# Optimization experiments

Measured on AMD Instinct MI355X. Metric: run time of the kernel, lower is better.

## Reference

```python
import jax, jax.numpy as jnp
import numpy as np

B, T, M, H = 64, 256, 512, 256  # batch, seq_len, d_model, lstm hidden


def setup_inputs() -> dict:
    key = jax.random.key(0)
    ks = jax.random.split(key, 10)
    s = 0.05  # weight init scale
    return {
        "enc_inputs": jax.random.normal(ks[0], (B, T, M), jnp.float32),
        "y": jax.random.normal(ks[1], (B, T, 1), jnp.float32),
        "Wd_w": jax.random.normal(ks[2], (M, 2 * H), jnp.float32) * s,  # W_d: Linear(2H, M)
        "Wd_b": jnp.zeros((M,), jnp.float32),
        "Ud_w": jax.random.normal(ks[3], (M, M), jnp.float32) * s,      # U_d: Linear(M, M, bias=False)
        "vd_w": jax.random.normal(ks[4], (1, M), jnp.float32) * s,      # v_d: Linear(M, 1, bias=False)
        "wt_w": jax.random.normal(ks[5], (1, M + 1), jnp.float32) * s,  # w_tilda: Linear(M+1, 1)
        "wt_b": jnp.zeros((1,), jnp.float32),
        "Wih": jax.random.normal(ks[6], (4 * H, 1), jnp.float32) * s,   # LSTMCell input weights
        "Whh": jax.random.normal(ks[7], (4 * H, H), jnp.float32) * s,   # LSTMCell hidden weights
        "bih": jnp.zeros((4 * H,), jnp.float32),
        "bhh": jnp.zeros((4 * H,), jnp.float32),
    }


def reference(enc_inputs, y, Wd_w, Wd_b, Ud_w, vd_w, wt_w, wt_b, Wih, Whh, bih, bhh):
    # U_d(enc_inputs) is loop-invariant -> hoist (same math as recomputing each step)
    y1 = jnp.einsum('btm,nm->btn', enc_inputs, Ud_w)  # [B,T,M]

    def step(carry, y_t):
        d, s = carry  # d = h_{t-1} [B,H], s = c'_{t-1} [B,H]
        x1 = jnp.concatenate([d, s], axis=1) @ Wd_w.T + Wd_b          # [B,M]
        z1 = jnp.tanh(x1[:, None, :] + y1)                            # [B,T,M]
        l_it = jnp.einsum('btm,m->bt', z1, vd_w[0])                   # [B,T]
        beta = jax.nn.softmax(l_it, axis=1)                           # softmax over encoder steps
        c_t = jnp.einsum('bt,btm->bm', beta, enc_inputs)              # [B,M]
        y_tilda = jnp.concatenate([c_t, y_t], axis=1) @ wt_w.T + wt_b # [B,1]
        # torch LSTMCell: gate order i, f, g, o
        gates = y_tilda @ Wih.T + bih + d @ Whh.T + bhh               # [B,4H]
        i, f, g, o = jnp.split(gates, 4, axis=1)
        s_new = jax.nn.sigmoid(f) * s + jax.nn.sigmoid(i) * jnp.tanh(g)
        d_new = jax.nn.sigmoid(o) * jnp.tanh(s_new)
        return (d_new, s_new), c_t

    b = enc_inputs.shape[0]
    init = (jnp.zeros((b, H), enc_inputs.dtype), jnp.zeros((b, H), enc_inputs.dtype))
    _, cs = jax.lax.scan(step, init, jnp.swapaxes(y, 0, 1))  # cs: [T,B,M]
    return jnp.sum(cs, axis=0)  # tgt = sum_t c_t, [B,M]
```

## Files before the change

kernel.cpp:

```cpp
#include <hip/hip_runtime.h>

typedef unsigned short u16;
typedef __attribute__((ext_vector_type(8))) short short8v;
typedef __attribute__((ext_vector_type(4))) float f32x4;

#define NB 64
#define NT 256
#define NM 512
#define NH 256

#define K2 2.8853900817779268f
#define LOG2E 1.4426950408889634f

__device__ __forceinline__ float bf2f(u16 u) {
  union { unsigned i; float f; } c; c.i = ((unsigned)u) << 16; return c.f;
}
__device__ __forceinline__ u16 f2bf(float f) {
  union { float fv; unsigned i; } c; c.fv = f;
  unsigned i = c.i;
  return (u16)((i + 0x7fffu + ((i >> 16) & 1u)) >> 16);
}
__device__ __forceinline__ float tanh_fast(float x) {
  return 1.0f - 2.0f * __builtin_amdgcn_rcpf(1.0f + __builtin_amdgcn_exp2f(K2 * x));
}
__device__ __forceinline__ float sigmoid_fast(float x) {
  return __builtin_amdgcn_rcpf(1.0f + __builtin_amdgcn_exp2f(-LOG2E * x));
}
__device__ __forceinline__ float uload(const float* p) {
  return __hip_atomic_load(p, __ATOMIC_RELAXED, __HIP_MEMORY_SCOPE_SYSTEM);
}
__device__ __forceinline__ void ustore(float* p, float v) {
  __hip_atomic_store(p, v, __ATOMIC_RELAXED, __HIP_MEMORY_SCOPE_SYSTEM);
}

__global__ void convert_f32_bf16(const float* __restrict__ in, u16* __restrict__ out, int n) {
  int i = blockIdx.x * blockDim.x + threadIdx.x;
  if (i < n) out[i] = f2bf(in[i]);
}

__global__ __launch_bounds__(256) void gemm_y1(const u16* __restrict__ A,
                                               const u16* __restrict__ Bm,
                                               u16* __restrict__ C) {
  const int w = threadIdx.x >> 6;
  const int l = threadIdx.x & 63;
  const int kg = l >> 4;
  const int r16 = l & 15;
  const int rowbase = blockIdx.x * 64 + w * 16;
  const int colbase = blockIdx.y * 64;
  const u16* ap = A + (size_t)(rowbase + r16) * 512 + kg * 8;
  f32x4 acc0 = {0,0,0,0}, acc1 = {0,0,0,0}, acc2 = {0,0,0,0}, acc3 = {0,0,0,0};
  for (int k = 0; k < 512; k += 32) {
    short8v af = *(const short8v*)(ap + k);
    const u16* bp = Bm + (size_t)(colbase + r16) * 512 + kg * 8 + k;
    short8v b0 = *(const short8v*)(bp);
    short8v b1 = *(const short8v*)(bp + 16 * 512);
    short8v b2 = *(const short8v*)(bp + 32 * 512);
    short8v b3 = *(const short8v*)(bp + 48 * 512);
    acc0 = __builtin_amdgcn_mfma_f32_16x16x32_bf16(af, b0, acc0, 0, 0, 0);
    acc1 = __builtin_amdgcn_mfma_f32_16x16x32_bf16(af, b1, acc1, 0, 0, 0);
    acc2 = __builtin_amdgcn_mfma_f32_16x16x32_bf16(af, b2, acc2, 0, 0, 0);
    ac3:
    acc3 = __builtin_amdgcn_mfma_f32_16x16x32_bf16(af, b3, acc3, 0, 0, 0);
  }
  const int rl = (l >> 4) * 4;
  #pragma unroll
  for (int j = 0; j < 4; ++j) {
    int r = rowbase + rl + j;
    C[(size_t)r * 512 + colbase +  0 + r16] = f2bf(K2 * acc0[j]);
    C[(size_t)r * 512 + colbase + 16 + r16] = f2bf(K2 * acc1[j]);
    C[(size_t)r * 512 + colbase + 32 + r16] = f2bf(K2 * acc2[j]);
    C[(size_t)r * 512 + colbase + 48 + r16] = f2bf(K2 * acc3[j]);
  }
}

__global__ __launch_bounds__(256) void wenc_kernel(const u16* __restrict__ encbf,
                                                   const float* __restrict__ wtw,
                                                   float* __restrict__ gwenc) {
  int b = blockIdx.x, te = threadIdx.x;
  const u16* ep = encbf + ((size_t)(b * NT + te)) * NM;
  float a = 0.0f;
  for (int c8 = 0; c8 < 64; ++c8) {
    short8v v = *(const short8v*)(ep + c8 * 8);
    #pragma unroll
    for (int jj = 0; jj < 8; ++jj) a = fmaf(bf2f((u16)v[jj]), wtw[c8 * 8 + jj], a);
  }
  gwenc[b * NT + te] = a;
}

__device__ __forceinline__ void batch_barrier(unsigned* c, unsigned target) {
  asm volatile("s_waitcnt vmcnt(0)" ::: "memory");
  __syncthreads();
  if (threadIdx.x == 0) {
    __hip_atomic_fetch_add(c, 1u, __ATOMIC_RELAXED, __HIP_MEMORY_SCOPE_SYSTEM);
    while (__hip_atomic_load(c, __ATOMIC_RELAXED, __HIP_MEMORY_SCOPE_SYSTEM) < target)
      __builtin_amdgcn_s_sleep(2);
  }
  __syncthreads();
}

__global__ __launch_bounds__(512) void attn_scan(
    const u16* __restrict__ y1bf,
    const u16* __restrict__ encbf,
    const u16* __restrict__ Wdbf,
    const u16* __restrict__ Whhbf,
    const float* __restrict__ Wd_b,
    const float* __restrict__ vd,
    const float* __restrict__ wtw,
    const float* __restrict__ wtb,
    const float* __restrict__ Wih,
    const float* __restrict__ bih,
    const float* __restrict__ bhh,
    const float* __restrict__ yin,
    const float* __restrict__ gwenc,
    float* __restrict__ gpx1,
    float* __restrict__ gl,
    float* __restrict__ gd,
    unsigned* __restrict__ ctr,
    float* __restrict__ out)
{
  extern __shared__ char ldsraw[];
  u16* y1_l  = (u16*)ldsraw;
  u16* enc_t = (u16*)(ldsraw + 65536);

  __shared__ float x1_l[NM];
  __shared__ float beta_l[NT];
  __shared__ float red_l[512];
  __shared__ float red2[16];
  __shared__ float dl[NH];
  __shared__ float gbuf[256];
  __shared__ float dnew_l[64], snew_l[64];
  __shared__ float w_enc_l[NT];

  const int tid = threadIdx.x;
  const int bid = blockIdx.x;
  const int xcd = bid & 7, ii = bid >> 3;
  const int b = (xcd << 3) | (ii >> 2);
  const int q = ii & 3;
  const int w = tid >> 6, l = tid & 63;

  {
    const u16* src = y1bf + ((size_t)(b * NT + q * 64) << 9);
    #pragma unroll
    for (int it = 0; it < 8; ++it) {
      int flat = it * 4096 + tid * 8;
      *(short8v*)(y1_l + flat) = *(const short8v*)(src + flat);
    }
  }
  #pragma unroll
  for (int it = 0; it < 8; ++it) {
    int flat = it * 4096 + tid * 8;
    int te = flat >> 7, ml0 = flat & 127;
    short8v v = *(const short8v*)(encbf + ((size_t)(b * NT + te) << 9) + q * 128 + ml0);
    int u = te >> 3, tlo = te & 7;
    #pragma unroll
    for (int jj = 0; jj < 8; ++jj) {
      int ml = ml0 + jj;
      enc_t[ml * 256 + ((u ^ (ml & 7)) << 3) + tlo] = (u16)v[jj];
    }
  }
  float vr[8];
  #pragma unroll
  for (int j = 0; j < 8; ++j) vr[j] = vd[l * 8 + j];
  float sv = 0.0f;
  #pragma unroll
  for (int j = 0; j < 8; ++j) sv += vr[j];
  #pragma unroll
  for (int off = 32; off > 0; off >>= 1) sv += __shfl_xor(sv, off, 64);
  const float Svd = sv;
  const float wdb_r = Wd_b[tid];
  const float wtw512 = wtw[NM];
  const float wtb0 = wtb[0];
  if (tid < 256) w_enc_l[tid] = gwenc[b * NT + tid];
  const int jrow = tid >> 1, half = tid & 1;
  const int r = ((jrow >> 6) << 8) + q * 64 + (jrow & 63);
  const float wih_r = Wih[r];
  const float bb_r = bih[r] + bhh[r];

  float s_reg = 0.0f;
  float out_acc = 0.0f;
  __syncthreads();

  unsigned* c0 = &ctr[b * 16 + 0];
  unsigned* c2 = &ctr[b * 16 + 1];

  #pragma unroll 1
  for (int t = 0; t < NT; ++t) {
    const unsigned tgt = 4u * (t + 1);
    if (tid < 256) dl[tid] = uload(&gd[(t & 1) * (NB * NH) + b * NH + tid]);
    {
      const float* p = gpx1 + b * 2048 + tid;
      float a0 = uload(p), a1 = uload(p + 512), a2 = uload(p + 1024), a3 = uload(p + 1536);
      x1_l[tid] = K2 * (wdb_r + ((a0 + a1) + (a2 + a3)));
    }
    __syncthreads();
    float xr[8];
    #pragma unroll
    for (int j = 0; j < 8; ++j) xr[j] = x1_l[l * 8 + j];
    #pragma unroll 1
    for (int i = 0; i < 8; ++i) {
      int te_loc = w * 8 + i;
      short8v yv = *(const short8v*)(y1_l + te_loc * 512 + l * 8);
      float a = 0.0f;
      #pragma unroll
      for (int j = 0; j < 8; ++j) {
        float e = __builtin_amdgcn_exp2f(xr[j] + bf2f((u16)yv[j]));
        a = fmaf(vr[j], __builtin_amdgcn_rcpf(1.0f + e), a);
      }
      #pragma unroll
      for (int off = 32; off > 0; off >>= 1) a += __shfl_xor(a, off, 64);
      if (l == 0) ustore(&gl[b * NT + q * 64 + te_loc], Svd - 2.0f * a);
    }
    batch_barrier(c0, tgt);

    float myl = -1e30f;
    if (tid < 256) myl = uload(&gl[b * NT + tid]);
    float m1 = myl;
    #pragma unroll
    for (int off = 32; off > 0; off >>= 1) m1 = fmaxf(m1, __shfl_xor(m1, off, 64));
    if (l == 0) red2[w] = m1;
    __syncthreads();
    const float mx = fmaxf(fmaxf(red2[0], red2[1]), fmaxf(red2[2], red2[3]));
    float pexp = 0.0f;
    if (tid < 256) pexp = __builtin_amdgcn_exp2f((myl - mx) * LOG2E);
    float s1 = pexp;
    #pragma unroll
    for (int off = 32; off > 0; off >>= 1) s1 += __shfl_xor(s1, off, 64);
    if (l == 0) red2[4 + w] = s1;
    __syncthreads();
    const float denom = (red2[4] + red2[5]) + (red2[6] + red2[7]);
    const float rden = __builtin_amdgcn_rcpf(denom);
    float mybeta = pexp * rden;
    if (tid < 256) beta_l[tid] = mybeta;
    float yp = (tid < 256) ? mybeta * w_enc_l[tid] : 0.0f;
    #pragma unroll
    for (int off = 32; off > 0; off >>= 1) yp += __shfl_xor(yp, off, 64);
    if (l == 0) red2[8 + w] = yp;
    __syncthreads();
    const float yt = (red2[8] + red2[9]) + (red2[10] + red2[11])
                   + wtw512 * yin[b * NT + t] + wtb0;
    {
      int tg = tid >> 7, ml = tid & 127;
      const u16* er = enc_t + ml * 256;
      int swz = ml & 7;
      float a = 0.0f;
      #pragma unroll
      for (int jj2 = 0; jj2 < 8; ++jj2) {
        int u = tg * 8 + jj2;
        short8v ev = *(const short8v*)(er + ((u ^ swz) << 3));
        #pragma unroll
        for (int jj = 0; jj < 8; ++jj)
          a = fmaf(bf2f((u16)ev[jj]), beta_l[(u << 3) + jj], a);
      }
      red_l[tid] = a;
    }
    {
      const u16* wr = Whhbf + (size_t)r * NH + half * 128;
      float a = 0.0f;
      #pragma unroll
      for (int c8 = 0; c8 < 16; ++c8) {
        short8v wv = *(const short8v*)(wr + c8 * 8);
        #pragma unroll
        for (int jj = 0; jj < 8; ++jj)
          a = fmaf(bf2f((u16)wv[jj]), dl[half * 128 + c8 * 8 + jj], a);
      }
      a += __shfl_xor(a, 1, 64);
      if (half == 0) gbuf[jrow] = a + yt * wih_r + bb_r;
    }
    __syncthreads();
    if (tid < 128) {
      float ctv = (red_l[tid] + red_l[128 + tid]) + (red_l[256 + tid] + red_l[384 + tid]);
      out_acc += ctv;
    }
    if (tid < 64) {
      float ig = sigmoid_fast(gbuf[tid]);
      float fg = sigmoid_fast(gbuf[64 + tid]);
      float gg = tanh_fast(gbuf[128 + tid]);
      float og = sigmoid_fast(gbuf[192 + tid]);
      float sn = fg * s_reg + ig * gg;
      s_reg = sn;
      float dn = og * tanh_fast(sn);
      ustore(&gd[((t + 1) & 1) * (NB * NH) + b * NH + q * 64 + tid], dn);
      dnew_l[tid] = dn;
      snew_l[tid] = sn;
    }
    __syncthreads();
    {
      const u16* wd_d = Wdbf + (size_t)tid * 512 + q * 64;
      const u16* wd_s = wd_d + 256;
      float a = 0.0f;
      #pragma unroll
      for (int c8 = 0; c8 < 8; ++c8) {
        short8v wv = *(const short8v*)(wd_d + c8 * 8);
        short8v wv2 = *(const short8v*)(wd_s + c8 * 8);
        #pragma unroll
        for (int jj = 0; jj < 8; ++jj) {
          a = fmaf(bf2f((u16)wv[jj]), dnew_l[c8 * 8 + jj], a);
          a = fmaf(bf2f((u16)wv2[jj]), snew_l[c8 * 8 + jj], a);
        }
      }
      ustore(&gpx1[b * 2048 + q * 512 + tid], a);
    }
    batch_barrier(c2, tgt);
  }
  if (tid < 128) out[b * NM + q * 128 + tid] = out_acc;
}

extern "C" void kernel_launch(void* const* d_in, const int* in_sizes, int n_in,
                              void* d_out, int out_size, void* d_ws, size_t ws_size,
                              hipStream_t stream) {
  const float* enc  = (const float*)d_in[0];
  const float* yin  = (const float*)d_in[1];
  const float* Wd_w = (const float*)d_in[2];
  const float* Wd_b = (const float*)d_in[3];
  const float* Ud_w = (const float*)d_in[4];
  const float* vd_w = (const float*)d_in[5];
  const float* wt_w = (const float*)d_in[6];
  const float* wt_b = (const float*)d_in[7];
  const float* Wih  = (const float*)d_in[8];
  const float* Whh  = (const float*)d_in[9];
  const float* bih  = (const float*)d_in[10];
  const float* bhh  = (const float*)d_in[11];

  char* ws = (char*)d_ws;
  u16*   y1bf  = (u16*)(ws);
  u16*   encbf = (u16*)(ws + 16777216);
  u16*   udbf  = (u16*)(ws + 33554432);
  u16*   wdbf  = (u16*)(ws + 34078720);
  u16*   whhbf = (u16*)(ws + 34603008);
  float* gpx1  = (float*)(ws + 35127296);
  float* gl    = (float*)(ws + 35651584);
  float* gd    = (float*)(ws + 35717120);
  unsigned* ctr = (unsigned*)(ws + 35848192);
  float* gwenc = (float*)(ws + 35852288);

  hipMemsetAsync(ws + 35127296, 0, 724992, stream);

  convert_f32_bf16<<<8388608 / 256, 256, 0, stream>>>(enc, encbf, 8388608);
  convert_f32_bf16<<<262144 / 256, 256, 0, stream>>>(Ud_w, udbf, 262144);
  convert_f32_bf16<<<262144 / 256, 256, 0, stream>>>(Wd_w, wdbf, 262144);
  convert_f32_bf16<<<262144 / 256, 256, 0, stream>>>(Whh, whhbf, 262144);
  gemm_y1<<<dim3(256, 8), 256, 0, stream>>>(encbf, udbf, y1bf);
  wenc_kernel<<<64, 256, 0, stream>>>(encbf, wt_w, gwenc);

  hipFuncSetAttribute((const void*)attn_scan,
                      hipFuncAttributeMaxDynamicSharedMemorySize, 131072);
  attn_scan<<<256, 512, 131072, stream>>>(y1bf, encbf, wdbf, whhbf, Wd_b, vd_w,
                                          wt_w, wt_b, Wih, bih, bhh, yin, gwenc,
                                          gpx1, gl, gd, ctr, (float*)d_out);
}
```

Before: 4.886 ms.

## Restructure recurrent scan with flag-based sync, partial softmax stats, 1024-thread blocks

Replaces the two atomic-counter batch barriers per step with per-quarter flag arrays polled through uncached loads. Instead of exchanging full attention logits, each block publishes local softmax max, sum and weighted-sum partials, so the context vector is rescaled locally and accumulated into the output with atomics at the end. Blocks grow to 1024 threads. Wd moves into LDS in a packed, swizzled layout, while y1 and enc are now read from global memory instead of staying resident in LDS. This adds global traffic every step and relies on cache-bypass ordering being correct.

```diff
diff --git a/kernel.cpp b/kernel.cpp
--- a/kernel.cpp
+++ b/kernel.cpp
@@ -1,8 +1,10 @@
 #include <hip/hip_runtime.h>
 
 typedef unsigned short u16;
+typedef unsigned int u32;
 typedef __attribute__((ext_vector_type(8))) short short8v;
 typedef __attribute__((ext_vector_type(4))) float f32x4;
+typedef __attribute__((ext_vector_type(4))) unsigned int u32x4;
 
 #define NB 64
 #define NT 256
@@ -20,17 +22,61 @@
   unsigned i = c.i;
   return (u16)((i + 0x7fffu + ((i >> 16) & 1u)) >> 16);
 }
+__device__ __forceinline__ float bits2f(u32 u) {
+  union { unsigned i; float f; } c; c.i = u; return c.f;
+}
 __device__ __forceinline__ float tanh_fast(float x) {
   return 1.0f - 2.0f * __builtin_amdgcn_rcpf(1.0f + __builtin_amdgcn_exp2f(K2 * x));
 }
 __device__ __forceinline__ float sigmoid_fast(float x) {
   return __builtin_amdgcn_rcpf(1.0f + __builtin_amdgcn_exp2f(-LOG2E * x));
 }
-__device__ __forceinline__ float uload(const float* p) {
-  return __hip_atomic_load(p, __ATOMIC_RELAXED, __HIP_MEMORY_SCOPE_SYSTEM);
-}
-__device__ __forceinline__ void ustore(float* p, float v) {
-  __hip_atomic_store(p, v, __ATOMIC_RELAXED, __HIP_MEMORY_SCOPE_SYSTEM);
+
+__device__ __forceinline__ float unc_ld1(const float* p) {
+  float r;
+  asm volatile("global_load_dword %0, %1, off sc0 sc1\n\ts_waitcnt vmcnt(0)"
+               : "=&v"(r) : "v"(p) : "memory");
+  return r;
+}
+__device__ __forceinline__ void unc_ld1x4(const float* p0, const float* p1,
+                                          const float* p2, const float* p3,
+                                          float& a0, float& a1, float& a2, float& a3) {
+  asm volatile(
+      "global_load_dword %0, %4, off sc0 sc1\n\t"
+      "global_load_dword %1, %5, off sc0 sc1\n\t"
+      "global_load_dword %2, %6, off sc0 sc1\n\t"
+      "global_load_dword %3, %7, off sc0 sc1\n\t"
+      "s_waitcnt vmcnt(0)"
+      : "=&v"(a0), "=&v"(a1), "=&v"(a2), "=&v"(a3)
+      : "v"(p0), "v"(p1), "v"(p2), "v"(p3)
+      : "memory");
+}
+__device__ __forceinline__ f32x4 unc_ld4f(const float* p) {
+  f32x4 r;
+  asm volatile("global_load_dwordx4 %0, %1, off sc0 sc1\n\ts_waitcnt vmcnt(0)"
+               : "=&v"(r) : "v"(p) : "memory");
+  return r;
+}
+__device__ __forceinline__ void unc_st1(float* p, float v) {
+  asm volatile("global_store_dword %0, %1, off sc0 sc1" :: "v"(p), "v"(v) : "memory");
+}
+__device__ __forceinline__ void unc_st1u(u32* p, u32 v) {
+  asm volatile("global_store_dword %0, %1, off sc0 sc1" :: "v"(p), "v"(v) : "memory");
+}
+__device__ __forceinline__ void unc_st4(float* p, f32x4 v) {
+  asm volatile("global_store_dwordx4 %0, %1, off sc0 sc1" :: "v"(p), "v"(v) : "memory");
+}
+__device__ __forceinline__ void drain_vmem() {
+  asm volatile("s_waitcnt vmcnt(0)" ::: "memory");
+}
+__device__ __forceinline__ void pollflags(const u32* p, u32 tg) {
+  for (;;) {
+    u32x4 f;
+    asm volatile("global_load_dwordx4 %0, %1, off sc0 sc1\n\ts_waitcnt vmcnt(0)"
+                 : "=&v"(f) : "v"(p) : "memory");
+    if (f[0] >= tg && f[1] >= tg && f[2] >= tg && f[3] >= tg) break;
+    __builtin_amdgcn_s_sleep(1);
+  }
 }
 
 __global__ void convert_f32_bf16(const float* __restrict__ in, u16* __restrict__ out, int n) {
@@ -59,13 +105,11 @@
     acc0 = __builtin_amdgcn_mfma_f32_16x16x32_bf16(af, b0, acc0, 0, 0, 0);
     acc1 = __builtin_amdgcn_mfma_f32_16x16x32_bf16(af, b1, acc1, 0, 0, 0);
     acc2 = __builtin_amdgcn_mfma_f32_16x16x32_bf16(af, b2, acc2, 0, 0, 0);
-    ac3:
     acc3 = __builtin_amdgcn_mfma_f32_16x16x32_bf16(af, b3, acc3, 0, 0, 0);
   }
-  const int rl = (l >> 4) * 4;
   #pragma unroll
   for (int j = 0; j < 4; ++j) {
-    int r = rowbase + rl + j;
+    int r = rowbase + (l >> 4) * 4 + j;
     C[(size_t)r * 512 + colbase +  0 + r16] = f2bf(K2 * acc0[j]);
     C[(size_t)r * 512 + colbase + 16 + r16] = f2bf(K2 * acc1[j]);
     C[(size_t)r * 512 + colbase + 32 + r16] = f2bf(K2 * acc2[j]);
@@ -87,22 +131,11 @@
   gwenc[b * NT + te] = a;
 }
 
-__device__ __forceinline__ void batch_barrier(unsigned* c, unsigned target) {
-  asm volatile("s_waitcnt vmcnt(0)" ::: "memory");
-  __syncthreads();
-  if (threadIdx.x == 0) {
-    __hip_atomic_fetch_add(c, 1u, __ATOMIC_RELAXED, __HIP_MEMORY_SCOPE_SYSTEM);
-    while (__hip_atomic_load(c, __ATOMIC_RELAXED, __HIP_MEMORY_SCOPE_SYSTEM) < target)
-      __builtin_amdgcn_s_sleep(2);
-  }
-  __syncthreads();
-}
-
-__global__ __launch_bounds__(512) void attn_scan(
+__global__ __launch_bounds__(1024, 1) void attn_scan(
     const u16* __restrict__ y1bf,
     const u16* __restrict__ encbf,
-    const u16* __restrict__ Wdbf,
-    const u16* __restrict__ Whhbf,
+    const u16* __restrict__ whhbf,
+    const u16* __restrict__ wdbf,
     const float* __restrict__ Wd_b,
     const float* __restrict__ vd,
     const float* __restrict__ wtw,
@@ -112,24 +145,25 @@
     const float* __restrict__ bhh,
     const float* __restrict__ yin,
     const float* __restrict__ gwenc,
-    float* __restrict__ gpx1,
-    float* __restrict__ gl,
-    float* __restrict__ gd,
-    unsigned* __restrict__ ctr,
+    float* __restrict__ gx,
+    float* __restrict__ st,
+    u32* __restrict__ flags,
     float* __restrict__ out)
 {
   extern __shared__ char ldsraw[];
-  u16* y1_l  = (u16*)ldsraw;
-  u16* enc_t = (u16*)(ldsraw + 65536);
+  u32* wdsl = (u32*)ldsraw;
 
   __shared__ float x1_l[NM];
-  __shared__ float beta_l[NT];
-  __shared__ float red_l[512];
-  __shared__ float red2[16];
-  __shared__ float dl[NH];
-  __shared__ float gbuf[256];
-  __shared__ float dnew_l[64], snew_l[64];
-  __shared__ float w_enc_l[NT];
+  __shared__ float d_l[NH];
+  __shared__ float ds_f[128];
+  __shared__ float l_sl[64];
+  __shared__ float e_sl[64];
+  __shared__ float whh_d_l[256];
+  __shared__ float wih_l[256];
+  __shared__ float bb_l[256];
+  __shared__ float wdb_l[NM];
+  __shared__ float wenc_sl[64];
+  __shared__ float ct_red[NM];
 
   const int tid = threadIdx.x;
   const int bid = blockIdx.x;
@@ -138,171 +172,200 @@
   const int q = ii & 3;
   const int w = tid >> 6, l = tid & 63;
 
-  {
-    const u16* src = y1bf + ((size_t)(b * NT + q * 64) << 9);
-    #pragma unroll
-    for (int it = 0; it < 8; ++it) {
-      int flat = it * 4096 + tid * 8;
-      *(short8v*)(y1_l + flat) = *(const short8v*)(src + flat);
-    }
-  }
-  #pragma unroll
-  for (int it = 0; it < 8; ++it) {
-    int flat = it * 4096 + tid * 8;
-    int te = flat >> 7, ml0 = flat & 127;
-    short8v v = *(const short8v*)(encbf + ((size_t)(b * NT + te) << 9) + q * 128 + ml0);
-    int u = te >> 3, tlo = te & 7;
-    #pragma unroll
-    for (int jj = 0; jj < 8; ++jj) {
-      int ml = ml0 + jj;
-      enc_t[ml * 256 + ((u ^ (ml & 7)) << 3) + tlo] = (u16)v[jj];
-    }
-  }
+  if (tid < 512) wdb_l[tid] = Wd_b[tid];
+  if (tid < 256) {
+    int g = tid >> 6, h = tid & 63;
+    int r = g * 256 + q * 64 + h;
+    wih_l[tid] = Wih[r];
+    bb_l[tid] = bih[r] + bhh[r];
+  }
+  if (tid < 64) wenc_sl[tid] = gwenc[b * NT + q * 64 + tid];
   float vr[8];
   #pragma unroll
-  for (int j = 0; j < 8; ++j) vr[j] = vd[l * 8 + j];
+  for (int j = 0; j < 8; ++j) vr[j] = vd[l + 64 * j];
   float sv = 0.0f;
   #pragma unroll
   for (int j = 0; j < 8; ++j) sv += vr[j];
   #pragma unroll
   for (int off = 32; off > 0; off >>= 1) sv += __shfl_xor(sv, off, 64);
   const float Svd = sv;
-  const float wdb_r = Wd_b[tid];
   const float wtw512 = wtw[NM];
   const float wtb0 = wtb[0];
-  if (tid < 256) w_enc_l[tid] = gwenc[b * NT + tid];
-  const int jrow = tid >> 1, half = tid & 1;
-  const int r = ((jrow >> 6) << 8) + q * 64 + (jrow & 63);
-  const float wih_r = Wih[r];
-  const float bb_r = bih[r] + bhh[r];
+
+  {
+    int m = tid >> 1, kh = tid & 1;
+    for (int j = 0; j < 32; ++j) {
+      int p = kh * 32 + j;
+      int k0 = 2 * p, k1 = 2 * p + 1;
+      int c0 = (k0 < 64) ? q * 64 + k0 : 256 + q * 64 + (k0 - 64);
+      int c1 = (k1 < 64) ? q * 64 + k1 : 256 + q * 64 + (k1 - 64);
+      u32 lo = wdbf[m * 512 + c0];
+      u32 hi = wdbf[m * 512 + c1];
+      int g = p >> 2, pg = g ^ (m & 15);
+      wdsl[m * 64 + pg * 4 + (p & 3)] = lo | (hi << 16);
+    }
+  }
 
   float s_reg = 0.0f;
   float out_acc = 0.0f;
   __syncthreads();
 
-  unsigned* c0 = &ctr[b * 16 + 0];
-  unsigned* c2 = &ctr[b * 16 + 1];
+  float* gxb = gx + b * 2304;
+  float* stb = st + b * 16;
+  u32* fS = flags + b * 32;
+  u32* fP = flags + b * 32 + 8;
 
   #pragma unroll 1
   for (int t = 0; t < NT; ++t) {
-    const unsigned tgt = 4u * (t + 1);
-    if (tid < 256) dl[tid] = uload(&gd[(t & 1) * (NB * NH) + b * NH + tid]);
+    pollflags(fP, (u32)t);
+    if (tid < 512) {
+      const float* p = gxb + tid;
+      float a0, a1, a2, a3;
+      unc_ld1x4(p, p + 576, p + 1152, p + 1728, a0, a1, a2, a3);
+      x1_l[tid] = K2 * (wdb_l[tid] + ((a0 + a1) + (a2 + a3)));
+    } else if (tid < 768) {
+      int h = tid - 512;
+      d_l[h] = unc_ld1(gxb + (h >> 6) * 576 + 512 + (h & 63));
+    }
+    __syncthreads();
+
+    float x1r[8];
+    #pragma unroll
+    for (int j = 0; j < 8; ++j) x1r[j] = x1_l[l + 64 * j];
     {
-      const float* p = gpx1 + b * 2048 + tid;
-      float a0 = uload(p), a1 = uload(p + 512), a2 = uload(p + 1024), a3 = uload(p + 1536);
-      x1_l[tid] = K2 * (wdb_r + ((a0 + a1) + (a2 + a3)));
+      const u16* yrow = y1bf + ((size_t)(b * NT + q * 64 + w * 4) << 9);
+      #pragma unroll
+      for (int i = 0; i < 4; ++i) {
+        float a = 0.0f;
+        #pragma unroll
+        for (int j = 0; j < 8; ++j) {
+          float yv = bf2f(yrow[i * 512 + l + 64 * j]);
+          float e = __builtin_amdgcn_exp2f(x1r[j] + yv);
+          a = fmaf(vr[j], __builtin_amdgcn_rcpf(1.0f + e), a);
+        }
+        #pragma unroll
+        for (int off = 32; off > 0; off >>= 1) a += __shfl_xor(a, off, 64);
+        if (l == i) l_sl[w * 4 + i] = Svd - 2.0f * a;
+      }
     }
     __syncthreads();
-    float xr[8];
-    #pragma unroll
-    for (int j = 0; j < 8; ++j) xr[j] = x1_l[l * 8 + j];
-    #pragma unroll 1
-    for (int i = 0; i < 8; ++i) {
-      int te_loc = w * 8 + i;
-      short8v yv = *(const short8v*)(y1_l + te_loc * 512 + l * 8);
+
+    if (w == 0) {
+      float v = l_sl[l];
+      float mq = v;
+      #pragma unroll
+      for (int off = 32; off > 0; off >>= 1) mq = fmaxf(mq, __shfl_xor(mq, off, 64));
+      float e = __builtin_amdgcn_exp2f((v - mq) * LOG2E);
+      e_sl[l] = e;
+      float sq = e, nq = e * wenc_sl[l];
+      #pragma unroll
+      for (int off = 32; off > 0; off >>= 1) {
+        sq += __shfl_xor(sq, off, 64);
+        nq += __shfl_xor(nq, off, 64);
+      }
+      if (l == 0) {
+        f32x4 quad = {mq, sq, nq, 0.0f};
+        unc_st4(stb + q * 4, quad);
+        drain_vmem();
+        unc_st1u(fS + q, (u32)(t + 1));
+      }
+    } else {
+      #pragma unroll 1
+      for (int pass = 0; pass < 2; ++pass) {
+        int slot = (pass == 0) ? (tid - 64) : (tid - 64 + 960);
+        if (pass == 1 && tid >= 128) break;
+        int rl = slot >> 2, kq = slot & 3;
+        const u16* wr = whhbf + (size_t)((rl >> 6) * 256 + q * 64 + (rl & 63)) * 256 + kq * 64;
+        float a = 0.0f;
+        #pragma unroll
+        for (int c8 = 0; c8 < 8; ++c8) {
+          short8v wv = *(const short8v*)(wr + c8 * 8);
+          #pragma unroll
+          for (int jj = 0; jj < 8; ++jj)
+            a = fmaf(bf2f((u16)wv[jj]), d_l[kq * 64 + c8 * 8 + jj], a);
+        }
+        a += __shfl_xor(a, 1, 64);
+        a += __shfl_xor(a, 2, 64);
+        if (kq == 0) whh_d_l[rl] = a;
+      }
+    }
+
+    pollflags(fS, (u32)(t + 1));
+    f32x4 s0 = unc_ld4f(stb + 0);
+    f32x4 s1 = unc_ld4f(stb + 4);
+    f32x4 s2 = unc_ld4f(stb + 8);
+    f32x4 s3 = unc_ld4f(stb + 12);
+    float mx = fmaxf(fmaxf(s0[0], s1[0]), fmaxf(s2[0], s3[0]));
+    float w0 = __builtin_amdgcn_exp2f((s0[0] - mx) * LOG2E);
+    float w1 = __builtin_amdgcn_exp2f((s1[0] - mx) * LOG2E);
+    float w2 = __builtin_amdgcn_exp2f((s2[0] - mx) * LOG2E);
+    float w3 = __builtin_amdgcn_exp2f((s3[0] - mx) * LOG2E);
+    float den = fmaf(s0[1], w0, fmaf(s1[1], w1, fmaf(s2[1], w2, s3[1] * w3)));
+    float rden = __builtin_amdgcn_rcpf(den);
+    float nsum = fmaf(s0[2], w0, fmaf(s1[2], w1, fmaf(s2[2], w2, s3[2] * w3)));
+    float yt = nsum * rden + wtw512 * yin[b * NT + t] + wtb0;
+    float wq = (q == 0) ? w0 : (q == 1) ? w1 : (q == 2) ? w2 : w3;
+    float sc_q = wq * rden;
+    __syncthreads();
+
+    if (tid < 64) {
+      int h = tid;
+      float gi = sigmoid_fast(whh_d_l[h]       + yt * wih_l[h]       + bb_l[h]);
+      float gf = sigmoid_fast(whh_d_l[64 + h]  + yt * wih_l[64 + h]  + bb_l[64 + h]);
+      float gg = tanh_fast   (whh_d_l[128 + h] + yt * wih_l[128 + h] + bb_l[128 + h]);
+      float go = sigmoid_fast(whh_d_l[192 + h] + yt * wih_l[192 + h] + bb_l[192 + h]);
+      float sn = gf * s_reg + gi * gg;
+      s_reg = sn;
+      float dn = go * tanh_fast(sn);
+      ds_f[h] = dn;
+      ds_f[64 + h] = sn;
+      unc_st1(gxb + q * 576 + 512 + h, dn);
+    }
+    __syncthreads();
+
+    {
+      int m = tid >> 1, kh = tid & 1;
       float a = 0.0f;
       #pragma unroll
-      for (int j = 0; j < 8; ++j) {
-        float e = __builtin_amdgcn_exp2f(xr[j] + bf2f((u16)yv[j]));
-        a = fmaf(vr[j], __builtin_amdgcn_rcpf(1.0f + e), a);
-      }
-      #pragma unroll
-      for (int off = 32; off > 0; off >>= 1) a += __shfl_xor(a, off, 64);
-      if (l == 0) ustore(&gl[b * NT + q * 64 + te_loc], Svd - 2.0f * a);
-    }
-    batch_barrier(c0, tgt);
-
-    float myl = -1e30f;
-    if (tid < 256) myl = uload(&gl[b * NT + tid]);
-    float m1 = myl;
-    #pragma unroll
-    for (int off = 32; off > 0; off >>= 1) m1 = fmaxf(m1, __shfl_xor(m1, off, 64));
-    if (l == 0) red2[w] = m1;
-    __syncthreads();
-    const float mx = fmaxf(fmaxf(red2[0], red2[1]), fmaxf(red2[2], red2[3]));
-    float pexp = 0.0f;
-    if (tid < 256) pexp = __builtin_amdgcn_exp2f((myl - mx) * LOG2E);
-    float s1 = pexp;
-    #pragma unroll
-    for (int off = 32; off > 0; off >>= 1) s1 += __shfl_xor(s1, off, 64);
-    if (l == 0) red2[4 + w] = s1;
-    __syncthreads();
-    const float denom = (red2[4] + red2[5]) + (red2[6] + red2[7]);
-    const float rden = __builtin_amdgcn_rcpf(denom);
-    float mybeta = pexp * rden;
-    if (tid < 256) beta_l[tid] = mybeta;
-    float yp = (tid < 256) ? mybeta * w_enc_l[tid] : 0.0f;
-    #pragma unroll
-    for (int off = 32; off > 0; off >>= 1) yp += __shfl_xor(yp, off, 64);
-    if (l == 0) red2[8 + w] = yp;
-    __syncthreads();
-    const float yt = (red2[8] + red2[9]) + (red2[10] + red2[11])
-                   + wtw512 * yin[b * NT + t] + wtb0;
-    {
-      int tg = tid >> 7, ml = tid & 127;
-      const u16* er = enc_t + ml * 256;
-      int swz = ml & 7;
-      float a = 0.0f;
-      #pragma unroll
-      for (int jj2 = 0; jj2 < 8; ++jj2) {
-        int u = tg * 8 + jj2;
-        short8v ev = *(const short8v*)(er + ((u ^ swz) << 3));
+      for (int i = 0; i < 8; ++i) {
+        int g = kh * 8 + i, pg = g ^ (m & 15);
+        u32x4 wv = *(const u32x4*)(wdsl + m * 64 + pg * 4);
+        const f32x4 dv0 = *(const f32x4*)(ds_f + kh * 64 + i * 8);
+        const f32x4 dv1 = *(const f32x4*)(ds_f + kh * 64 + i * 8 + 4);
         #pragma unroll
-        for (int jj = 0; jj < 8; ++jj)
-          a = fmaf(bf2f((u16)ev[jj]), beta_l[(u << 3) + jj], a);
-      }
-      red_l[tid] = a;
-    }
-    {
-      const u16* wr = Whhbf + (size_t)r * NH + half * 128;
-      float a = 0.0f;
-      #pragma unroll
-      for (int c8 = 0; c8 < 16; ++c8) {
-        short8v wv = *(const short8v*)(wr + c8 * 8);
-        #pragma unroll
-        for (int jj = 0; jj < 8; ++jj)
-          a = fmaf(bf2f((u16)wv[jj]), dl[half * 128 + c8 * 8 + jj], a);
+        for (int n = 0; n < 4; ++n) {
+          u32 v = wv[n];
+          float wlo = bits2f(v << 16);
+          float whi = bits2f(v & 0xffff0000u);
+          float dlo = (n < 2) ? dv0[2 * n] : dv1[2 * n - 4];
+          float dhi = (n < 2) ? dv0[2 * n + 1] : dv1[2 * n - 3];
+          a = fmaf(wlo, dlo, a);
+          a = fmaf(whi, dhi, a);
+        }
       }
       a += __shfl_xor(a, 1, 64);
-      if (half == 0) gbuf[jrow] = a + yt * wih_r + bb_r;
-    }
+      if (kh == 0) unc_st1(gxb + q * 576 + m, a);
+    }
+    drain_vmem();
     __syncthreads();
-    if (tid < 128) {
-      float ctv = (red_l[tid] + red_l[128 + tid]) + (red_l[256 + tid] + red_l[384 + tid]);
-      out_acc += ctv;
-    }
-    if (tid < 64) {
-      float ig = sigmoid_fast(gbuf[tid]);
-      float fg = sigmoid_fast(gbuf[64 + tid]);
-      float gg = tanh_fast(gbuf[128 + tid]);
-      float og = sigmoid_fast(gbuf[192 + tid]);
-      float sn = fg * s_reg + ig * gg;
-      s_reg = sn;
-      float dn = og * tanh_fast(sn);
-      ustore(&gd[((t + 1) & 1) * (NB * NH) + b * NH + q * 64 + tid], dn);
-      dnew_l[tid] = dn;
-      snew_l[tid] = sn;
-    }
-    __syncthreads();
+    if (tid == 0) unc_st1u(fP + q, (u32)(t + 1));
+
     {
-      const u16* wd_d = Wdbf + (size_t)tid * 512 + q * 64;
-      const u16* wd_s = wd_d + 256;
+      int c = tid >> 9, m = tid & 511;
+      const u16* ep = encbf + ((size_t)(b * NT + q * 64 + c * 32) << 9) + m;
       float a = 0.0f;
-      #pragma unroll
-      for (int c8 = 0; c8 < 8; ++c8) {
-        short8v wv = *(const short8v*)(wd_d + c8 * 8);
-        short8v wv2 = *(const short8v*)(wd_s + c8 * 8);
-        #pragma unroll
-        for (int jj = 0; jj < 8; ++jj) {
-          a = fmaf(bf2f((u16)wv[jj]), dnew_l[c8 * 8 + jj], a);
-          a = fmaf(bf2f((u16)wv2[jj]), snew_l[c8 * 8 + jj], a);
-        }
-      }
-      ustore(&gpx1[b * 2048 + q * 512 + tid], a);
-    }
-    batch_barrier(c2, tgt);
-  }
-  if (tid < 128) out[b * NM + q * 128 + tid] = out_acc;
+      #pragma unroll 8
+      for (int i = 0; i < 32; ++i)
+        a = fmaf(bf2f(ep[(size_t)i * 512]), e_sl[c * 32 + i], a);
+      if (c) ct_red[m] = a;
+      __syncthreads();
+      if (!c) out_acc += (a + ct_red[m]) * sc_q;
+    }
+  }
+
+  if (tid < 512)
+    __hip_atomic_fetch_add(&out[b * NM + tid], out_acc,
+                           __ATOMIC_RELAXED, __HIP_MEMORY_SCOPE_SYSTEM);
 }
 
 extern "C" void kernel_launch(void* const* d_in, const int* in_sizes, int n_in,
@@ -327,13 +390,13 @@
   u16*   udbf  = (u16*)(ws + 33554432);
   u16*   wdbf  = (u16*)(ws + 34078720);
   u16*   whhbf = (u16*)(ws + 34603008);
-  float* gpx1  = (float*)(ws + 35127296);
-  float* gl    = (float*)(ws + 35651584);
-  float* gd    = (float*)(ws + 35717120);
-  unsigned* ctr = (unsigned*)(ws + 35848192);
-  float* gwenc = (float*)(ws + 35852288);
-
-  hipMemsetAsync(ws + 35127296, 0, 724992, stream);
+  float* gwenc = (float*)(ws + 35127296);
+  float* gx    = (float*)(ws + 35192832);
+  float* st    = (float*)(ws + 35782656);
+  u32*   flags = (u32*)(ws + 35786752);
+
+  hipMemsetAsync(ws + 35192832, 0, 602112, stream);
+  hipMemsetAsync(d_out, 0, (size_t)out_size * sizeof(float), stream);
 
   convert_f32_bf16<<<8388608 / 256, 256, 0, stream>>>(enc, encbf, 8388608);
   convert_f32_bf16<<<262144 / 256, 256, 0, stream>>>(Ud_w, udbf, 262144);
@@ -344,7 +407,7 @@
 
   hipFuncSetAttribute((const void*)attn_scan,
                       hipFuncAttributeMaxDynamicSharedMemorySize, 131072);
-  attn_scan<<<256, 512, 131072, stream>>>(y1bf, encbf, wdbf, whhbf, Wd_b, vd_w,
-                                          wt_w, wt_b, Wih, bih, bhh, yin, gwenc,
-                                          gpx1, gl, gd, ctr, (float*)d_out);
-}
+  attn_scan<<<256, 1024, 131072, stream>>>(y1bf, encbf, whhbf, wdbf, Wd_b, vd_w,
+                                           wt_w, wt_b, Wih, bih, bhh, yin, gwenc,
+                                           gx, st, flags, (float*)d_out);
+}
```

Result: faster. 4.420 ms (-9.5%).
